# Performance work log

Measured on AMD Instinct MI355X. Metric: run time of the kernel, lower is better.

The kernel has to match this reference:

```python
import jax, jax.numpy as jnp
import numpy as np

MARGIN = 0.1
CURV = 1.0
NUM_SAMPLES_PER_CLASS = 64
NUM_NEGATIVES = 8
NUM_CLASSES = 105
B, D, H, W, Z = 1, 32, 128, 128, 128


def _lorentz_dist(x, y, curv):
    # x, y: [..., D] space components of Lorentz-model points.
    # time component: sqrt(1/curv + |x|^2); Lorentz inner: <x,y> - x_t*y_t
    xt = jnp.sqrt(1.0 / curv + jnp.sum(x * x, axis=-1))
    yt = jnp.sqrt(1.0 / curv + jnp.sum(y * y, axis=-1))
    inner = jnp.sum(x * y, axis=-1) - xt * yt
    arg = jnp.maximum(-curv * inner, 1.0 + 1e-7)  # acosh domain guard
    return jnp.arccosh(arg) / jnp.sqrt(curv)


def setup_inputs() -> dict:
    key = jax.random.key(0)
    k1, k2 = jax.random.split(key)
    voxel_emb = jax.random.normal(k1, (B, D, H, W, Z), dtype=jnp.float32)
    label_emb = jax.random.normal(k2, (NUM_CLASSES, D), dtype=jnp.float32)

    rng = np.random.default_rng(0)
    labels_np = rng.integers(0, NUM_CLASSES, size=(B, H, W, Z)).astype(np.int64)
    flat = labels_np.reshape(-1)

    # Per-class anchor sampling (host-side index generation, as in torch randperm).
    sampled_idx, sampled_cls = [], []
    for c in np.unique(flat):
        idx = np.flatnonzero(flat == c)
        n = min(len(idx), NUM_SAMPLES_PER_CLASS)
        pick = rng.permutation(len(idx))[:n]
        sampled_idx.append(idx[pick])
        sampled_cls.append(np.full(n, c, dtype=np.int64))
    sampled_indices = np.concatenate(sampled_idx)
    sampled_classes = np.concatenate(sampled_cls)
    K = sampled_indices.shape[0]

    # Per-anchor negative class sampling: NUM_NEGATIVES random classes != true class.
    scores = rng.random((K, NUM_CLASSES))
    scores[np.arange(K), sampled_classes] = 2.0  # exclude own class
    neg_class_indices = np.argsort(scores, axis=1)[:, :NUM_NEGATIVES].astype(np.int64)

    return {
        "voxel_emb": voxel_emb,
        "labels": jnp.asarray(labels_np),
        "label_emb": label_emb,
        "sampled_indices": jnp.asarray(sampled_indices),
        "sampled_classes": jnp.asarray(sampled_classes),
        "neg_class_indices": jnp.asarray(neg_class_indices),
    }


def reference(voxel_emb, labels, label_emb, sampled_indices, sampled_classes, neg_class_indices):
    voxel_emb = voxel_emb.astype(jnp.float32)
    label_emb = label_emb.astype(jnp.float32)
    # [B,D,H,W,Z] -> [B*H*W*Z, D]
    voxel_flat = jnp.transpose(voxel_emb, (0, 2, 3, 4, 1)).reshape(-1, D)

    anchors = voxel_flat[sampled_indices]            # [K, D]
    positives = label_emb[sampled_classes]           # [K, D]
    d_pos = _lorentz_dist(anchors, positives, CURV)  # [K]

    negatives = label_emb[neg_class_indices]         # [K, M, D]
    d_neg = _lorentz_dist(anchors[:, None, :], negatives, CURV)  # [K, M]

    triplet = jnp.maximum(MARGIN + d_pos[:, None] - d_neg, 0.0)  # [K, M]
    # per-anchor mean over negatives, then mean over anchors (matches loop/valid_count)
    return jnp.mean(jnp.mean(triplet, axis=1))
```

## Files before the change

kernel.cpp:

```cpp
#include <hip/hip_runtime.h>
#include <math.h>


#define NUM_NEG 8

__device__ __forceinline__ float lorentz_dist_row(const float x[32], float xt,
                                                  const float* __restrict__ yrow) {
    float yy = 0.f, dot = 0.f;
#pragma unroll
    for (int q = 0; q < 8; ++q) {
        float4 y4 = reinterpret_cast<const float4*>(yrow)[q];
        yy  = fmaf(y4.x, y4.x, yy);
        yy  = fmaf(y4.y, y4.y, yy);
        yy  = fmaf(y4.z, y4.z, yy);
        yy  = fmaf(y4.w, y4.w, yy);
        dot = fmaf(y4.x, x[q * 4 + 0], dot);
        dot = fmaf(y4.y, x[q * 4 + 1], dot);
        dot = fmaf(y4.z, x[q * 4 + 2], dot);
        dot = fmaf(y4.w, x[q * 4 + 3], dot);
    }
    float yt  = sqrtf(1.0f + yy);
    float arg = fmaxf(fmaf(xt, yt, -dot), 1.0f + 1e-7f);
    return acoshf(arg);
}

__global__ __launch_bounds__(256)
void lorentz_pair_kernel(const float* __restrict__ voxel,
                         const float* __restrict__ label,
                         const int* __restrict__ sidx,
                         const int* __restrict__ scls,
                         const int* __restrict__ negc,
                         float* __restrict__ partial,
                         int K, int S) {
    int t = blockIdx.x * 256 + threadIdx.x;
    float tri = 0.f;
    if (t < K * NUM_NEG) {
        int a = t >> 3;
        int idx = sidx[a];
        float x[32];
#pragma unroll
        for (int d = 0; d < 32; ++d)
            x[d] = voxel[(size_t)d * (size_t)S + (size_t)idx];

        float xx = 0.f;
#pragma unroll
        for (int d = 0; d < 32; ++d) xx = fmaf(x[d], x[d], xx);
        float xt = sqrtf(1.0f + xx);

        float dpos = lorentz_dist_row(x, xt, label + (size_t)scls[a] * 32);
        float dneg = lorentz_dist_row(x, xt, label + (size_t)negc[t] * 32);
        tri = fmaxf(0.1f + dpos - dneg, 0.f);
    }

#pragma unroll
    for (int o = 32; o > 0; o >>= 1) tri += __shfl_down(tri, o);

    __shared__ float ws[4];
    int lane = threadIdx.x & 63, w = threadIdx.x >> 6;
    if (lane == 0) ws[w] = tri;
    __syncthreads();
    if (threadIdx.x == 0)
        partial[blockIdx.x] = ws[0] + ws[1] + ws[2] + ws[3];
}

__global__ __launch_bounds__(64)
void lorentz_reduce_kernel(const float* __restrict__ partial, int nb,
                           float* __restrict__ out, float scale) {
    float s = 0.f;
    for (int i = threadIdx.x; i < nb; i += 64) s += partial[i];
#pragma unroll
    for (int o = 32; o > 0; o >>= 1) s += __shfl_down(s, o);
    if (threadIdx.x == 0) out[0] = s * scale;
}

extern "C" void kernel_launch(void* const* d_in, const int* in_sizes, int n_in,
                              void* d_out, int out_size, void* d_ws, size_t ws_size,
                              hipStream_t stream) {
    const float* voxel = (const float*)d_in[0];
    const float* label = (const float*)d_in[2];
    const int* sidx    = (const int*)d_in[3];
    const int* scls    = (const int*)d_in[4];
    const int* negc    = (const int*)d_in[5];

    int K = in_sizes[3];
    int S = in_sizes[1];

    float* partial = (float*)d_ws;
    float* out     = (float*)d_out;

    int total = K * NUM_NEG;
    int nb = (total + 255) / 256;
    lorentz_pair_kernel<<<nb, 256, 0, stream>>>(voxel, label, sidx, scls, negc,
                                                partial, K, S);
    lorentz_reduce_kernel<<<1, 64, 0, stream>>>(partial, nb, out,
                                                1.0f / (float)(K * NUM_NEG));
}
```

Measured before the change: 12.28 us.

## Fuse final reduction into pair kernel via flagged atomic slots

Removes the second reduce kernel launch. Each block publishes its partial sum together with a ready flag into a 64-bit slot using atomicExch. Block 0 then spin-waits on every slot, consuming and resetting each one before doing the final reduction. This saves a launch and its gap, but block 0 busy-waits on other blocks, which assumes they all become resident or get scheduled; with K about 6720 there are about 210 blocks, which should fit on the device.

```diff
diff --git a/kernel.cpp b/kernel.cpp
--- a/kernel.cpp
+++ b/kernel.cpp
@@ -25,13 +25,14 @@
 }
 
 __global__ __launch_bounds__(256)
-void lorentz_pair_kernel(const float* __restrict__ voxel,
-                         const float* __restrict__ label,
-                         const int* __restrict__ sidx,
-                         const int* __restrict__ scls,
-                         const int* __restrict__ negc,
-                         float* __restrict__ partial,
-                         int K, int S) {
+void lorentz_fused_kernel(const float* __restrict__ voxel,
+                          const float* __restrict__ label,
+                          const int* __restrict__ sidx,
+                          const int* __restrict__ scls,
+                          const int* __restrict__ negc,
+                          unsigned long long* __restrict__ slots,
+                          float* __restrict__ out,
+                          int K, int S, int nb, float scale) {
     int t = blockIdx.x * 256 + threadIdx.x;
     float tri = 0.f;
     if (t < K * NUM_NEG) {
@@ -55,22 +56,31 @@
 #pragma unroll
     for (int o = 32; o > 0; o >>= 1) tri += __shfl_down(tri, o);
 
-    __shared__ float ws[4];
+    __shared__ float ws4[4];
     int lane = threadIdx.x & 63, w = threadIdx.x >> 6;
-    if (lane == 0) ws[w] = tri;
+    if (lane == 0) ws4[w] = tri;
     __syncthreads();
-    if (threadIdx.x == 0)
-        partial[blockIdx.x] = ws[0] + ws[1] + ws[2] + ws[3];
-}
 
-__global__ __launch_bounds__(64)
-void lorentz_reduce_kernel(const float* __restrict__ partial, int nb,
-                           float* __restrict__ out, float scale) {
-    float s = 0.f;
-    for (int i = threadIdx.x; i < nb; i += 64) s += partial[i];
+    if (threadIdx.x == 0) {
+        float p = ws4[0] + ws4[1] + ws4[2] + ws4[3];
+        unsigned long long payload =
+            (1ULL << 32) | (unsigned long long)__float_as_uint(p);
+        atomicExch(&slots[blockIdx.x], payload);
+    }
+
+    if (blockIdx.x == 0 && threadIdx.x < 64) {
+        float s = 0.f;
+        for (int i = threadIdx.x; i < nb; i += 64) {
+            unsigned long long v;
+            do {
+                v = atomicExch(&slots[i], 0ULL);
+            } while ((v >> 32) != 1ULL);
+            s += __uint_as_float((unsigned)(v & 0xffffffffULL));
+        }
 #pragma unroll
-    for (int o = 32; o > 0; o >>= 1) s += __shfl_down(s, o);
-    if (threadIdx.x == 0) out[0] = s * scale;
+        for (int o = 32; o > 0; o >>= 1) s += __shfl_down(s, o);
+        if (threadIdx.x == 0) out[0] = s * scale;
+    }
 }
 
 extern "C" void kernel_launch(void* const* d_in, const int* in_sizes, int n_in,
@@ -85,13 +95,12 @@
     int K = in_sizes[3];
     int S = in_sizes[1];
 
-    float* partial = (float*)d_ws;
-    float* out     = (float*)d_out;
+    unsigned long long* slots = (unsigned long long*)d_ws;
+    float* out = (float*)d_out;
 
     int total = K * NUM_NEG;
     int nb = (total + 255) / 256;
-    lorentz_pair_kernel<<<nb, 256, 0, stream>>>(voxel, label, sidx, scls, negc,
-                                                partial, K, S);
-    lorentz_reduce_kernel<<<1, 64, 0, stream>>>(partial, nb, out,
-                                                1.0f / (float)(K * NUM_NEG));
+    lorentz_fused_kernel<<<nb, 256, 0, stream>>>(voxel, label, sidx, scls, negc,
+                                                 slots, out, K, S, nb,
+                                                 1.0f / (float)total);
 }
```

After: 11.30 us. -8.0%, faster.
